# Kernel tuning notes

Hardware: AMD Instinct MI355X
Metric: run time of the kernel (lower is better)

## Reference

```python
import jax, jax.numpy as jnp
import numpy as np

B, N, E, H, L = 32, 128, 128, 8, 4      # graphs, nodes/graph, emb, heads, layers
ATOM, BOND, K, M = 64, 15, 32, 16384    # atom_dim, bond_dim, rbf_K, n_edges
CUTOFF = 5.0
DH = E // H


def _ln(x, g, b):
    mu = x.mean(-1, keepdims=True)
    var = ((x - mu) ** 2).mean(-1, keepdims=True)
    return (x - mu) / jnp.sqrt(var + 1e-5) * g + b


def setup_inputs() -> dict:
    key = jax.random.key(0)
    ks = iter(jax.random.split(key, 40))
    def rn(shape, s=1.0):
        return jax.random.normal(next(ks), shape, jnp.float32) * s
    inp = {}
    inp["x"] = rn((B * N, ATOM))
    inp["ei"] = jax.random.randint(next(ks), (2, M), 0, B * N, jnp.int32)
    bf = rn((M, BOND))
    dist = jax.random.uniform(next(ks), (M, 1), jnp.float32, 0.0, CUTOFF)
    inp["ea"] = jnp.concatenate([bf, dist], axis=1)  # last col = distance
    inp["pos"] = rn((B * N, 3), 2.0)
    inp["batch"] = jnp.repeat(jnp.arange(B, dtype=jnp.int32), N)  # contiguous equal-size graphs
    s = 0.02
    inp["Wproj"] = rn((ATOM, E), s); inp["bproj"] = jnp.zeros((E,), jnp.float32)
    EIN = BOND + K
    inp["Wlin"] = rn((EIN, E * E), s); inp["blin"] = jnp.zeros((E * E,), jnp.float32)
    inp["g_en"] = jnp.ones((E,), jnp.float32); inp["b_en"] = jnp.zeros((E,), jnp.float32)
    for nm in ["Wq", "Wk", "Wv", "Wo"]:
        inp[nm] = rn((L, E, E), s)
    for nm in ["bq", "bk", "bv", "bo"]:
        inp[nm] = jnp.zeros((L, E), jnp.float32)
    inp["g1"] = jnp.ones((L, E), jnp.float32); inp["b1"] = jnp.zeros((L, E), jnp.float32)
    inp["W1"] = rn((L, E, 2 * E), s); inp["bf1"] = jnp.zeros((L, 2 * E), jnp.float32)
    inp["W2"] = rn((L, 2 * E, E), s); inp["bf2"] = jnp.zeros((L, E), jnp.float32)
    inp["g2"] = jnp.ones((L, E), jnp.float32); inp["b2"] = jnp.zeros((L, E), jnp.float32)
    return inp


def reference(x, ei, ea, pos, batch, Wproj, bproj, Wlin, blin, g_en, b_en,
              Wq, bq, Wk, bk, Wv, bv, Wo, bo, g1, b1, W1, bf1, W2, bf2, g2, b2):
    # node projection
    h = x @ Wproj + bproj                              # [BN, E]
    # GaussianRBF on last edge-attr column
    d = jnp.clip(ea[:, -1], 0.0, 10.0)
    centers = jnp.linspace(0.0, CUTOFF, K)
    gamma = (CUTOFF / (K - 1)) ** -2
    rbf = jnp.exp(-gamma * (d[:, None] - centers) ** 2)  # [M, K]
    ea2 = jnp.concatenate([ea[:, :-1], rbf], axis=1)     # [M, BOND+K]
    # EdgeNetwork: gather -> per-edge matvec -> scatter-add -> LN
    m = (ea2 @ Wlin + blin).reshape(M, E, E)             # [M, E, E]
    msg = jnp.einsum('mef,mf->me', m, h[ei[1]])          # [M, E]
    agg = jnp.zeros_like(h).at[ei[0]].add(msg)
    h = _ln(h + agg, g_en, b_en)
    # batch-to-dense (equal-size contiguous graphs -> reshape)
    xp = h.reshape(B, N, E)
    pb = pos.reshape(B, N, 3)
    d2 = jnp.sum((pb[:, :, None, :] - pb[:, None, :, :]) ** 2, axis=-1)  # [B, N, N]
    db = jnp.where(d2 > 0, jnp.sqrt(jnp.where(d2 > 0, d2, 1.0)), 0.0)    # cdist
    mask = jnp.ones((B, N), bool)
    inv_sqrt_dh = 1.0 / np.sqrt(DH)
    for l in range(L):
        q = (xp @ Wq[l] + bq[l]).reshape(B, N, H, DH)
        k = (xp @ Wk[l] + bk[l]).reshape(B, N, H, DH)
        v = (xp @ Wv[l] + bv[l]).reshape(B, N, H, DH)
        sc = jnp.einsum('bihd,bjhd->bhij', q, k) * inv_sqrt_dh + db[:, None]
        sc = jnp.clip(sc, -10.0, 10.0)
        sc = jnp.where(mask[:, None, None, :], sc, -jnp.inf)
        a = jax.nn.softmax(sc, axis=-1)
        o = jnp.einsum('bhij,bjhd->bihd', a, v).reshape(B, N, E)
        att = o @ Wo[l] + bo[l]
        x1 = _ln(xp + att, g1[l], b1[l])
        ff = jax.nn.relu(x1 @ W1[l] + bf1[l]) @ W2[l] + bf2[l]
        xp = _ln(x1 + ff, g2[l], b2[l])
    mf = mask.astype(xp.dtype)[:, :, None]
    return (xp * mf).sum(1) / (mf.sum(1) + 1e-8)      # [B, E]
```

## Files before the change

kernel.cpp:

```cpp
#include <hip/hip_runtime.h>


typedef __attribute__((ext_vector_type(8))) short bf16x8;
typedef __attribute__((ext_vector_type(4))) float f32x4;
#define MFMA16(a, b, c) __builtin_amdgcn_mfma_f32_16x16x32_bf16(a, b, c, 0, 0, 0)

__device__ inline unsigned short f2bf(float f) {
  unsigned u = __float_as_uint(f);
  u = (u + 0x7FFF + ((u >> 16) & 1)) >> 16;
  return (unsigned short)u;
}
__device__ inline unsigned pack2(float a, float b) {
  return (unsigned)f2bf(a) | ((unsigned)f2bf(b) << 16);
}

__global__ __launch_bounds__(256) void k_setup(
    const float* __restrict__ x, const float* __restrict__ Wproj,
    const float* __restrict__ bproj, float* __restrict__ h,
    unsigned short* __restrict__ hb,
    const float* __restrict__ ea, float* __restrict__ ea2,
    const float* __restrict__ Wlin, const float* __restrict__ blin,
    unsigned short* __restrict__ wb,
    const float* __restrict__ Wq, const float* __restrict__ Wk,
    const float* __restrict__ Wv, const float* __restrict__ bq,
    const float* __restrict__ bk, const float* __restrict__ bv,
    unsigned short* __restrict__ qkvt, float* __restrict__ qkvb,
    const float* __restrict__ Wo, unsigned short* __restrict__ wot,
    const float* __restrict__ W1, unsigned short* __restrict__ w1t,
    const float* __restrict__ W2, unsigned short* __restrict__ w2t,
    float* __restrict__ agg,
    const float* __restrict__ pos, float* __restrict__ db) {
  __shared__ float xs[2][64];
  int blk = blockIdx.x, t = threadIdx.x;
  if (blk < 2048) {
    int sub = t >> 7, e = t & 127;
    int n = blk * 2 + sub;
    if (e < 64) xs[sub][e] = x[n * 64 + e];
    __syncthreads();
    float acc = bproj[e];
#pragma unroll
    for (int a = 0; a < 64; a++) acc += xs[sub][a] * Wproj[a * 128 + e];
    h[n * 128 + e] = acc;
    hb[n * 128 + e] = f2bf(acc);
    return;
  }
  int idx = (blk - 2048) * 256 + t;
  if (idx < 524288) { agg[idx] = 0.0f; return; }
  idx -= 524288;
  if (idx < 786432) {
    int m = idx / 48, c = idx % 48;
    float v;
    if (c < 15) {
      v = ea[m * 16 + c];
    } else if (c < 47) {
      int i = c - 15;
      float d = fminf(10.0f, fmaxf(0.0f, ea[m * 16 + 15]));
      float diff = d - 5.0f * (float)i / 31.0f;
      v = __expf(-38.44f * diff * diff);
    } else {
      v = 1.0f;
    }
    ea2[m * 48 + c] = v;
    return;
  }
  idx -= 786432;
  if (idx < 786432) {
    float v = (idx < 770048) ? Wlin[idx] : blin[idx - 770048];
    wb[idx] = f2bf(v);
    return;
  }
  idx -= 786432;
  if (idx < 196608) {
    int l = idx / 49152, r = idx % 49152;
    int j = r / 128, a = r % 128;
    int jj = j & 127;
    const float* W = (j < 128) ? Wq : (j < 256) ? Wk : Wv;
    qkvt[idx] = f2bf(W[l * 16384 + a * 128 + jj]);
    if (a == 0) {
      const float* bb = (j < 128) ? bq : (j < 256) ? bk : bv;
      qkvb[l * 384 + j] = bb[l * 128 + jj];
    }
    return;
  }
  idx -= 196608;
  if (idx < 65536) {
    int l = idx / 16384, r = idx % 16384;
    int a = r / 128, j = r % 128;
    wot[l * 16384 + j * 128 + a] = f2bf(Wo[idx]);
    return;
  }
  idx -= 65536;
  if (idx < 131072) {
    int l = idx / 32768, r = idx % 32768;
    int a = r / 256, j = r % 256;
    w1t[l * 32768 + j * 128 + a] = f2bf(W1[idx]);
    return;
  }
  idx -= 131072;
  if (idx < 131072) {
    int l = idx / 32768, r = idx % 32768;
    int a = r / 128, j = r % 128;
    w2t[l * 32768 + j * 256 + a] = f2bf(W2[idx]);
    return;
  }
  idx -= 131072;
  {
    int j = idx & 127, i2 = (idx >> 7) & 127, b = idx >> 14;
    float x0 = pos[(b * 128 + i2) * 3 + 0];
    float y0 = pos[(b * 128 + i2) * 3 + 1];
    float z0 = pos[(b * 128 + i2) * 3 + 2];
    float dx = x0 - pos[(b * 128 + j) * 3 + 0];
    float dy = y0 - pos[(b * 128 + j) * 3 + 1];
    float dz = z0 - pos[(b * 128 + j) * 3 + 2];
    float d2 = dx * dx + dy * dy + dz * dz;
    db[b * 16384 + i2 * 128 + j] = (d2 > 0.0f) ? sqrtf(d2) : 0.0f;
  }
}

__global__ __launch_bounds__(256) void k_edge(const float* __restrict__ ea2,
    const int* __restrict__ ei, const unsigned short* __restrict__ hbf,
    const unsigned short* __restrict__ wb, float* __restrict__ agg) {
  __shared__ unsigned short hs[8192];
  __shared__ float et[64][48];
  __shared__ unsigned short Bs[16384];
  __shared__ int srcs[64], dsts[64];
  int t = threadIdx.x, m0 = blockIdx.x * 64;
  if (t < 64) { srcs[t] = ei[16384 + m0 + t]; dsts[t] = ei[m0 + t]; }
  __syncthreads();
  uint4* hs4 = (uint4*)hs;
#pragma unroll
  for (int i = 0; i < 4; i++) {
    int q = t + i * 256;
    int row = q >> 4, ch = q & 15;
    hs4[row * 16 + (ch ^ (row & 7))] = ((const uint4*)(hbf + (size_t)srcs[row] * 128))[ch];
  }
#pragma unroll
  for (int i = 0; i < 12; i++) {
    int p = t + i * 256;
    int mi = p / 48, c = p % 48;
    et[mi][c] = ea2[(size_t)(m0 + mi) * 48 + c];
  }
  int w = t >> 6, l = t & 63, lr = l & 15, lg = l >> 4;
  float msg[2][4][4] = {};
  const f32x4 zf = {0.f, 0.f, 0.f, 0.f};
  uint4* Bs4 = (uint4*)Bs;
  for (int c = 0; c < 48; c++) {
    __syncthreads();
#pragma unroll
    for (int i = 0; i < 8; i++) {
      int q = t + i * 256;
      int row = q >> 4, ch = q & 15;
      Bs4[row * 16 + (ch ^ (row & 7))] =
          ((const uint4*)(wb + (size_t)c * 16384 + row * 128))[ch];
    }
    __syncthreads();
    f32x4 pacc[2][4];
#pragma unroll
    for (int s = 0; s < 4; s++) {
      bf16x8 af[2];
#pragma unroll
      for (int e2 = 0; e2 < 2; e2++) {
        int er = w * 32 + e2 * 16 + lr;
        int ch = (s * 4 + lg) ^ (er & 7);
        af[e2] = *(const bf16x8*)&Bs[(er * 16 + ch) * 8];
      }
#pragma unroll
      for (int n = 0; n < 4; n++) {
        int nr = n * 16 + lr;
        int ch = (s * 4 + lg) ^ (nr & 7);
        bf16x8 bfr = *(const bf16x8*)&hs[(nr * 16 + ch) * 8];
        if (s == 0) {
          pacc[0][n] = MFMA16(af[0], bfr, zf);
          pacc[1][n] = MFMA16(af[1], bfr, zf);
        } else {
          pacc[0][n] = MFMA16(af[0], bfr, pacc[0][n]);
          pacc[1][n] = MFMA16(af[1], bfr, pacc[1][n]);
        }
      }
    }
#pragma unroll
    for (int n = 0; n < 4; n++) {
      float am = et[n * 16 + lr][c];
#pragma unroll
      for (int e2 = 0; e2 < 2; e2++)
#pragma unroll
        for (int r = 0; r < 4; r++)
          msg[e2][n][r] += am * pacc[e2][n][r];
    }
  }
#pragma unroll
  for (int n = 0; n < 4; n++) {
    int dst = dsts[n * 16 + lr];
#pragma unroll
    for (int e2 = 0; e2 < 2; e2++) {
      int e0 = w * 32 + e2 * 16 + lg * 4;
#pragma unroll
      for (int r = 0; r < 4; r++)
        atomicAdd(&agg[(size_t)dst * 128 + e0 + r], msg[e2][n][r]);
    }
  }
}

__global__ __launch_bounds__(256) void k_lnqkv(const float* __restrict__ agg,
    const float* __restrict__ hbuf, const float* __restrict__ g_en,
    const float* __restrict__ b_en, float* __restrict__ xp,
    const unsigned short* __restrict__ qkvt, const float* __restrict__ qkvb,
    float* __restrict__ qkv) {
  __shared__ unsigned short As[8192];
  __shared__ unsigned short Bs[16384];
  int t = threadIdx.x, m0 = blockIdx.x * 64;
  int w = t >> 6, l = t & 63, lr = l & 15, lg = l >> 4;
  float ge0 = g_en[2 * l], ge1 = g_en[2 * l + 1];
  float be0 = b_en[2 * l], be1 = b_en[2 * l + 1];
  for (int i = 0; i < 16; i++) {
    int r = i * 4 + w;
    float2 av = ((const float2*)(agg + (size_t)(m0 + r) * 128))[l];
    float2 hv = ((const float2*)(hbuf + (size_t)(m0 + r) * 128))[l];
    float v0 = av.x + hv.x, v1 = av.y + hv.y;
    float s = v0 + v1, s2 = v0 * v0 + v1 * v1;
#pragma unroll
    for (int o = 1; o < 64; o <<= 1) { s += __shfl_xor(s, o); s2 += __shfl_xor(s2, o); }
    float mu = s * (1.0f / 128.0f);
    float var = fmaxf(s2 * (1.0f / 128.0f) - mu * mu, 0.0f);
    float inv = rsqrtf(var + 1e-5f);
    float o0 = (v0 - mu) * inv * ge0 + be0;
    float o1 = (v1 - mu) * inv * ge1 + be1;
    ((float2*)(xp + (size_t)(m0 + r) * 128))[l] = make_float2(o0, o1);
    ((unsigned*)As)[(r * 16 + ((l >> 2) ^ (r & 7))) * 4 + (l & 3)] = pack2(o0, o1);
  }
  uint4* Bs4 = (uint4*)Bs;
  for (int cchunk = 0; cchunk < 3; cchunk++) {
    __syncthreads();
#pragma unroll
    for (int i = 0; i < 8; i++) {
      int q = t + i * 256;
      int row = q >> 4, ch = q & 15;
      Bs4[row * 16 + (ch ^ (row & 7))] =
          ((const uint4*)(qkvt + (size_t)(cchunk * 128 + row) * 128))[ch];
    }
    __syncthreads();
    f32x4 acc[2][4];
#pragma unroll
    for (int e2 = 0; e2 < 2; e2++)
#pragma unroll
      for (int n = 0; n < 4; n++) acc[e2][n] = (f32x4){0.f, 0.f, 0.f, 0.f};
#pragma unroll
    for (int s = 0; s < 4; s++) {
      bf16x8 af[2];
#pragma unroll
      for (int e2 = 0; e2 < 2; e2++) {
        int er = w * 32 + e2 * 16 + lr;
        int ch = (s * 4 + lg) ^ (er & 7);
        af[e2] = *(const bf16x8*)&Bs[(er * 16 + ch) * 8];
      }
#pragma unroll
      for (int n = 0; n < 4; n++) {
        int nr = n * 16 + lr;
        int ch = (s * 4 + lg) ^ (nr & 7);
        bf16x8 bfr = *(const bf16x8*)&As[(nr * 16 + ch) * 8];
        acc[0][n] = MFMA16(af[0], bfr, acc[0][n]);
        acc[1][n] = MFMA16(af[1], bfr, acc[1][n]);
      }
    }
#pragma unroll
    for (int e2 = 0; e2 < 2; e2++) {
      int e0 = cchunk * 128 + w * 32 + e2 * 16 + lg * 4;
      float4 bb = *(const float4*)&qkvb[e0];
#pragma unroll
      for (int n = 0; n < 4; n++) {
        int node = m0 + n * 16 + lr;
        float4 ov;
#pragma unroll
        for (int r = 0; r < 4; r++) ((float*)&ov)[r] = acc[e2][n][r] + ((const float*)&bb)[r];
        *(float4*)&qkv[(size_t)node * 384 + e0] = ov;
      }
    }
  }
}

__global__ __launch_bounds__(128) void k_attn(const float* __restrict__ qkv,
    const float* __restrict__ db, float* __restrict__ oatt) {
  __shared__ float ks[128][16], vs[128][16];
  int bh = blockIdx.x, b = bh >> 3, h = bh & 7;
  int i = threadIdx.x;
  int node = b * 128 + i;
  const float4* kr = (const float4*)(qkv + (size_t)node * 384 + 128 + h * 16);
  const float4* vr = (const float4*)(qkv + (size_t)node * 384 + 256 + h * 16);
#pragma unroll
  for (int d4 = 0; d4 < 4; d4++) {
    *(float4*)&ks[i][d4 * 4] = kr[d4];
    *(float4*)&vs[i][d4 * 4] = vr[d4];
  }
  float qr[16];
  const float4* qp = (const float4*)(qkv + (size_t)node * 384 + h * 16);
#pragma unroll
  for (int d4 = 0; d4 < 4; d4++) *(float4*)&qr[d4 * 4] = qp[d4];
  __syncthreads();
  const float4* dbr = (const float4*)(db + b * 16384 + i * 128);
  float rsum = 0.0f, o[16] = {};
  for (int j4 = 0; j4 < 32; j4++) {
    float4 dv = dbr[j4];
#pragma unroll
    for (int u = 0; u < 4; u++) {
      int j = j4 * 4 + u;
      float s = 0.0f;
#pragma unroll
      for (int d = 0; d < 16; d++) s += qr[d] * ks[j][d];
      s = s * 0.25f + ((const float*)&dv)[u];
      s = fminf(10.0f, fmaxf(-10.0f, s));
      float p = __expf(s);
      rsum += p;
#pragma unroll
      for (int d = 0; d < 16; d++) o[d] += p * vs[j][d];
    }
  }
  float r = 1.0f / rsum;
  float* op = oatt + (size_t)node * 128 + h * 16;
#pragma unroll
  for (int d4 = 0; d4 < 4; d4++)
    *(float4*)&op[d4 * 4] = make_float4(o[d4 * 4] * r, o[d4 * 4 + 1] * r, o[d4 * 4 + 2] * r, o[d4 * 4 + 3] * r);
}

template <int QKV>
__global__ __launch_bounds__(256) void k_loqkv(
    const float* __restrict__ oatt, float* __restrict__ xp,
    const unsigned short* __restrict__ wot, const float* __restrict__ bo,
    const float* __restrict__ g1, const float* __restrict__ b1,
    const unsigned short* __restrict__ w1t, const float* __restrict__ bf1,
    const unsigned short* __restrict__ w2t, const float* __restrict__ bf2,
    const float* __restrict__ g2, const float* __restrict__ b2,
    const unsigned short* __restrict__ qkvtn, const float* __restrict__ qkvbn,
    float* __restrict__ qkv) {
  __shared__ unsigned short ffs[16384];
  __shared__ unsigned short x1s[8192];
  __shared__ unsigned short Bs[16384];
  __shared__ float red[2][4][64];
  int t = threadIdx.x;
  int m0 = blockIdx.x << 6;
  int w = t >> 6, l = t & 63, lr = l & 15, lg = l >> 4;

  {
    uint4* a4 = (uint4*)ffs;
#pragma unroll
    for (int i = 0; i < 4; i++) {
      int q = t + i * 256;
      int row = q >> 4, ch = q & 15;
      const float* ap = oatt + (size_t)(m0 + row) * 128 + ch * 8;
      float4 fa = *(const float4*)ap;
      float4 fb = *(const float4*)(ap + 4);
      uint4 pk;
      pk.x = pack2(fa.x, fa.y); pk.y = pack2(fa.z, fa.w);
      pk.z = pack2(fb.x, fb.y); pk.w = pack2(fb.z, fb.w);
      a4[row * 16 + (ch ^ (row & 7))] = pk;
    }
    uint4* b4p = (uint4*)Bs;
#pragma unroll
    for (int i = 0; i < 8; i++) {
      int q = t + i * 256;
      int row = q >> 4, ch = q & 15;
      b4p[row * 16 + (ch ^ (row & 7))] = *((const uint4*)(wot + (size_t)row * 128) + ch);
    }
  }
  __syncthreads();
  f32x4 acc[2][4];
#pragma unroll
  for (int et = 0; et < 2; et++)
#pragma unroll
    for (int n = 0; n < 4; n++) acc[et][n] = (f32x4){0.f, 0.f, 0.f, 0.f};
#pragma unroll
  for (int s = 0; s < 4; s++) {
    bf16x8 af[2];
#pragma unroll
    for (int et = 0; et < 2; et++) {
      int er = w * 32 + et * 16 + lr;
      int ch = (s * 4 + lg) ^ (er & 7);
      af[et] = *(const bf16x8*)&Bs[(er * 16 + ch) * 8];
    }
#pragma unroll
    for (int n = 0; n < 4; n++) {
      int nr = n * 16 + lr;
      int ch = (s * 4 + lg) ^ (nr & 7);
      bf16x8 bfr = *(const bf16x8*)&ffs[(nr * 16 + ch) * 8];
      acc[0][n] = MFMA16(af[0], bfr, acc[0][n]);
      acc[1][n] = MFMA16(af[1], bfr, acc[1][n]);
    }
  }
  float v1[2][4][4];
  {
    int e0 = w * 32 + lg * 4;
    float4 bo4[2] = { *(const float4*)&bo[e0], *(const float4*)&bo[e0 + 16] };
#pragma unroll
    for (int et = 0; et < 2; et++)
#pragma unroll
      for (int n = 0; n < 4; n++) {
        int node = m0 + n * 16 + lr;
        float4 rv = *(const float4*)&xp[(size_t)node * 128 + e0 + et * 16];
#pragma unroll
        for (int r = 0; r < 4; r++)
          v1[et][n][r] = acc[et][n][r] + ((const float*)&bo4[et])[r] + ((const float*)&rv)[r];
      }
    float s[4], s2[4];
#pragma unroll
    for (int n = 0; n < 4; n++) {
      float a = 0, b2s = 0;
#pragma unroll
      for (int et = 0; et < 2; et++)
#pragma unroll
        for (int r = 0; r < 4; r++) { a += v1[et][n][r]; b2s += v1[et][n][r] * v1[et][n][r]; }
      s[n] = a; s2[n] = b2s;
    }
#pragma unroll
    for (int off = 16; off < 64; off <<= 1)
#pragma unroll
      for (int n = 0; n < 4; n++) { s[n] += __shfl_xor(s[n], off); s2[n] += __shfl_xor(s2[n], off); }
    if (l < 16) {
#pragma unroll
      for (int n = 0; n < 4; n++) { red[0][w][n * 16 + lr] = s[n]; red[1][w][n * 16 + lr] = s2[n]; }
    }
    __syncthreads();
    float4 g4[2] = { *(const float4*)&g1[e0], *(const float4*)&g1[e0 + 16] };
    float4 bb4[2] = { *(const float4*)&b1[e0], *(const float4*)&b1[e0 + 16] };
#pragma unroll
    for (int n = 0; n < 4; n++) {
      int nloc = n * 16 + lr;
      float ts  = red[0][0][nloc] + red[0][1][nloc] + red[0][2][nloc] + red[0][3][nloc];
      float ts2 = red[1][0][nloc] + red[1][1][nloc] + red[1][2][nloc] + red[1][3][nloc];
      float mu = ts * (1.0f / 128.0f);
      float var = fmaxf(ts2 * (1.0f / 128.0f) - mu * mu, 0.0f);
      float inv = rsqrtf(var + 1e-5f);
#pragma unroll
      for (int et = 0; et < 2; et++) {
#pragma unroll
        for (int r = 0; r < 4; r++)
          v1[et][n][r] = (v1[et][n][r] - mu) * inv * ((const float*)&g4[et])[r] + ((const float*)&bb4[et])[r];
        int ch = w * 4 + et * 2 + (lg >> 1);
        uint2 pk;
        pk.x = pack2(v1[et][n][0], v1[et][n][1]);
        pk.y = pack2(v1[et][n][2], v1[et][n][3]);
        *(uint2*)&x1s[(nloc * 16 + (ch ^ (nloc & 7))) * 8 + (lg & 1) * 4] = pk;
      }
    }
  }
  __syncthreads();

  for (int ct = 0; ct < 2; ct++) {
    if (ct) __syncthreads();
    uint4* b4p = (uint4*)Bs;
#pragma unroll
    for (int i = 0; i < 8; i++) {
      int q = t + i * 256;
      int row = q >> 4, ch = q & 15;
      b4p[row * 16 + (ch ^ (row & 7))] =
          *((const uint4*)(w1t + (size_t)(ct * 128 + row) * 128) + ch);
    }
    __syncthreads();
#pragma unroll
    for (int et = 0; et < 2; et++)
#pragma unroll
      for (int n = 0; n < 4; n++) acc[et][n] = (f32x4){0.f, 0.f, 0.f, 0.f};
#pragma unroll
    for (int s = 0; s < 4; s++) {
      bf16x8 af[2];
#pragma unroll
      for (int et = 0; et < 2; et++) {
        int er = w * 32 + et * 16 + lr;
        int ch = (s * 4 + lg) ^ (er & 7);
        af[et] = *(const bf16x8*)&Bs[(er * 16 + ch) * 8];
      }
#pragma unroll
      for (int n = 0; n < 4; n++) {
        int nr = n * 16 + lr;
        int ch = (s * 4 + lg) ^ (nr & 7);
        bf16x8 bfr = *(const bf16x8*)&x1s[(nr * 16 + ch) * 8];
        acc[0][n] = MFMA16(af[0], bfr, acc[0][n]);
        acc[1][n] = MFMA16(af[1], bfr, acc[1][n]);
      }
    }
    int e0 = w * 32 + lg * 4;
    float4 bb0 = *(const float4*)&bf1[ct * 128 + e0];
    float4 bb1 = *(const float4*)&bf1[ct * 128 + e0 + 16];
#pragma unroll
    for (int et = 0; et < 2; et++) {
      const float* bbp = et ? (const float*)&bb1 : (const float*)&bb0;
#pragma unroll
      for (int n = 0; n < 4; n++) {
        int nloc = n * 16 + lr;
        float f0 = fmaxf(acc[et][n][0] + bbp[0], 0.0f);
        float f1 = fmaxf(acc[et][n][1] + bbp[1], 0.0f);
        float f2 = fmaxf(acc[et][n][2] + bbp[2], 0.0f);
        float f3 = fmaxf(acc[et][n][3] + bbp[3], 0.0f);
        int cg = ct * 16 + w * 4 + et * 2 + (lg >> 1);
        uint2 pk;
        pk.x = pack2(f0, f1);
        pk.y = pack2(f2, f3);
        *(uint2*)&ffs[(nloc * 32 + (cg ^ (nloc & 7))) * 8 + (lg & 1) * 4] = pk;
      }
    }
  }
  __syncthreads();

  f32x4 acc3[2][4];
#pragma unroll
  for (int et = 0; et < 2; et++)
#pragma unroll
    for (int n = 0; n < 4; n++) acc3[et][n] = (f32x4){0.f, 0.f, 0.f, 0.f};
  for (int kc = 0; kc < 2; kc++) {
    if (kc) __syncthreads();
    uint4* b4p = (uint4*)Bs;
#pragma unroll
    for (int i = 0; i < 8; i++) {
      int q = t + i * 256;
      int row = q >> 4, ch = q & 15;
      b4p[row * 16 + (ch ^ (row & 7))] =
          *((const uint4*)(w2t + (size_t)row * 256 + kc * 128) + ch);
    }
    __syncthreads();
#pragma unroll
    for (int s = 0; s < 4; s++) {
      bf16x8 af[2];
#pragma unroll
      for (int et = 0; et < 2; et++) {
        int er = w * 32 + et * 16 + lr;
        int ch = (s * 4 + lg) ^ (er & 7);
        af[et] = *(const bf16x8*)&Bs[(er * 16 + ch) * 8];
      }
#pragma unroll
      for (int n = 0; n < 4; n++) {
        int nr = n * 16 + lr;
        int gch = kc * 16 + s * 4 + lg;
        bf16x8 bfr = *(const bf16x8*)&ffs[(nr * 32 + (gch ^ (nr & 7))) * 8];
        acc3[0][n] = MFMA16(af[0], bfr, acc3[0][n]);
        acc3[1][n] = MFMA16(af[1], bfr, acc3[1][n]);
      }
    }
  }
  {
    int e0 = w * 32 + lg * 4;
    float4 bo4[2] = { *(const float4*)&bf2[e0], *(const float4*)&bf2[e0 + 16] };
    float v2[2][4][4];
#pragma unroll
    for (int et = 0; et < 2; et++)
#pragma unroll
      for (int n = 0; n < 4; n++)
#pragma unroll
        for (int r = 0; r < 4; r++)
          v2[et][n][r] = acc3[et][n][r] + ((const float*)&bo4[et])[r] + v1[et][n][r];
    float s[4], s2[4];
#pragma unroll
    for (int n = 0; n < 4; n++) {
      float a = 0, b2s = 0;
#pragma unroll
      for (int et = 0; et < 2; et++)
#pragma unroll
        for (int r = 0; r < 4; r++) { a += v2[et][n][r]; b2s += v2[et][n][r] * v2[et][n][r]; }
      s[n] = a; s2[n] = b2s;
    }
#pragma unroll
    for (int off = 16; off < 64; off <<= 1)
#pragma unroll
      for (int n = 0; n < 4; n++) { s[n] += __shfl_xor(s[n], off); s2[n] += __shfl_xor(s2[n], off); }
    __syncthreads();
    if (l < 16) {
#pragma unroll
      for (int n = 0; n < 4; n++) { red[0][w][n * 16 + lr] = s[n]; red[1][w][n * 16 + lr] = s2[n]; }
    }
    __syncthreads();
    float4 g4[2] = { *(const float4*)&g2[e0], *(const float4*)&g2[e0 + 16] };
    float4 bb4[2] = { *(const float4*)&b2[e0], *(const float4*)&b2[e0 + 16] };
#pragma unroll
    for (int n = 0; n < 4; n++) {
      int nloc = n * 16 + lr;
      float ts  = red[0][0][nloc] + red[0][1][nloc] + red[0][2][nloc] + red[0][3][nloc];
      float ts2 = red[1][0][nloc] + red[1][1][nloc] + red[1][2][nloc] + red[1][3][nloc];
      float mu = ts * (1.0f / 128.0f);
      float var = fmaxf(ts2 * (1.0f / 128.0f) - mu * mu, 0.0f);
      float inv = rsqrtf(var + 1e-5f);
      int node = m0 + nloc;
#pragma unroll
      for (int et = 0; et < 2; et++) {
        float4 ov;
#pragma unroll
        for (int r = 0; r < 4; r++)
          ((float*)&ov)[r] = (v2[et][n][r] - mu) * inv * ((const float*)&g4[et])[r] + ((const float*)&bb4[et])[r];
        *(float4*)&xp[(size_t)node * 128 + e0 + et * 16] = ov;
        if (QKV) {
          int ch = w * 4 + et * 2 + (lg >> 1);
          uint2 pk;
          pk.x = pack2(((float*)&ov)[0], ((float*)&ov)[1]);
          pk.y = pack2(((float*)&ov)[2], ((float*)&ov)[3]);
          *(uint2*)&x1s[(nloc * 16 + (ch ^ (nloc & 7))) * 8 + (lg & 1) * 4] = pk;
        }
      }
    }
  }

  if (QKV) {
    uint4* Bs4 = (uint4*)Bs;
    for (int cchunk = 0; cchunk < 3; cchunk++) {
      __syncthreads();
#pragma unroll
      for (int i = 0; i < 8; i++) {
        int q = t + i * 256;
        int row = q >> 4, ch = q & 15;
        Bs4[row * 16 + (ch ^ (row & 7))] =
            ((const uint4*)(qkvtn + (size_t)(cchunk * 128 + row) * 128))[ch];
      }
      __syncthreads();
      f32x4 qa[2][4];
#pragma unroll
      for (int e2 = 0; e2 < 2; e2++)
#pragma unroll
        for (int n = 0; n < 4; n++) qa[e2][n] = (f32x4){0.f, 0.f, 0.f, 0.f};
#pragma unroll
      for (int s = 0; s < 4; s++) {
        bf16x8 af[2];
#pragma unroll
        for (int e2 = 0; e2 < 2; e2++) {
          int er = w * 32 + e2 * 16 + lr;
          int ch = (s * 4 + lg) ^ (er & 7);
          af[e2] = *(const bf16x8*)&Bs[(er * 16 + ch) * 8];
        }
#pragma unroll
        for (int n = 0; n < 4; n++) {
          int nr = n * 16 + lr;
          int ch = (s * 4 + lg) ^ (nr & 7);
          bf16x8 bfr = *(const bf16x8*)&x1s[(nr * 16 + ch) * 8];
          qa[0][n] = MFMA16(af[0], bfr, qa[0][n]);
          qa[1][n] = MFMA16(af[1], bfr, qa[1][n]);
        }
      }
#pragma unroll
      for (int e2 = 0; e2 < 2; e2++) {
        int e0 = cchunk * 128 + w * 32 + e2 * 16 + lg * 4;
        float4 bb = *(const float4*)&qkvbn[e0];
#pragma unroll
        for (int n = 0; n < 4; n++) {
          int node = m0 + n * 16 + lr;
          float4 ov;
#pragma unroll
          for (int r = 0; r < 4; r++) ((float*)&ov)[r] = qa[e2][n][r] + ((const float*)&bb)[r];
          *(float4*)&qkv[(size_t)node * 384 + e0] = ov;
        }
      }
    }
  }
}

__global__ __launch_bounds__(128) void k_pool(const float* __restrict__ xp, float* __restrict__ out) {
  int b = blockIdx.x, e = threadIdx.x;
  float s = 0.0f;
  for (int n = 0; n < 128; n++) s += xp[(b * 128 + n) * 128 + e];
  out[b * 128 + e] = s * (1.0f / 128.0f);
}

extern "C" void kernel_launch(void* const* d_in, const int* in_sizes, int n_in,
                              void* d_out, int out_size, void* d_ws, size_t ws_size,
                              hipStream_t stream) {
  const float* x     = (const float*)d_in[0];
  const int*   ei    = (const int*)  d_in[1];
  const float* ea    = (const float*)d_in[2];
  const float* pos   = (const float*)d_in[3];
  const float* Wproj = (const float*)d_in[5];
  const float* bproj = (const float*)d_in[6];
  const float* Wlin  = (const float*)d_in[7];
  const float* blin  = (const float*)d_in[8];
  const float* g_en  = (const float*)d_in[9];
  const float* b_en  = (const float*)d_in[10];
  const float* Wq    = (const float*)d_in[11];
  const float* Wk    = (const float*)d_in[12];
  const float* Wv    = (const float*)d_in[13];
  const float* Wo    = (const float*)d_in[14];
  const float* bq    = (const float*)d_in[15];
  const float* bk    = (const float*)d_in[16];
  const float* bv    = (const float*)d_in[17];
  const float* bo    = (const float*)d_in[18];
  const float* g1    = (const float*)d_in[19];
  const float* b1    = (const float*)d_in[20];
  const float* W1    = (const float*)d_in[21];
  const float* bf1   = (const float*)d_in[22];
  const float* W2    = (const float*)d_in[23];
  const float* bf2   = (const float*)d_in[24];
  const float* g2    = (const float*)d_in[25];
  const float* b2    = (const float*)d_in[26];

  float* ws = (float*)d_ws;
  float* ea2  = ws;
  float* hbuf = ea2  + 786432;
  float* agg  = hbuf + 524288;
  unsigned short* hbf  = (unsigned short*)(agg + 524288);
  unsigned short* wbf  = hbf + 524288;
  unsigned short* qkvt = wbf + 786432;
  unsigned short* wot  = qkvt + 196608;
  unsigned short* w1t  = wot + 65536;
  unsigned short* w2t  = w1t + 131072;
  float* qkvb = (float*)(w2t + 131072);
  float* db   = qkvb + 1536;
  float* xp   = db   + 524288;
  float* qkv  = xp   + 524288;
  float* oatt = qkv  + 1572864;

  k_setup<<<14336, 256, 0, stream>>>(x, Wproj, bproj, hbuf, hbf,
      ea, ea2, Wlin, blin, wbf, Wq, Wk, Wv, bq, bk, bv, qkvt, qkvb,
      Wo, wot, W1, w1t, W2, w2t, agg, pos, db);
  k_edge<<<256, 256, 0, stream>>>(ea2, ei, hbf, wbf, agg);
  k_lnqkv<<<64, 256, 0, stream>>>(agg, hbuf, g_en, b_en, xp, qkvt, qkvb, qkv);

  for (int l = 0; l < 4; l++) {
    k_attn<<<256, 128, 0, stream>>>(qkv, db, oatt);
    if (l < 3) {
      k_loqkv<1><<<64, 256, 0, stream>>>(oatt, xp,
          wot + l * 16384, bo + l * 128, g1 + l * 128, b1 + l * 128,
          w1t + l * 32768, bf1 + l * 256,
          w2t + l * 32768, bf2 + l * 128, g2 + l * 128, b2 + l * 128,
          qkvt + (l + 1) * 49152, qkvb + (l + 1) * 384, qkv);
    } else {
      k_loqkv<0><<<64, 256, 0, stream>>>(oatt, xp,
          wot + l * 16384, bo + l * 128, g1 + l * 128, b1 + l * 128,
          w1t + l * 32768, bf1 + l * 256,
          w2t + l * 32768, bf2 + l * 128, g2 + l * 128, b2 + l * 128,
          nullptr, nullptr, nullptr);
    }
  }

  k_pool<<<32, 128, 0, stream>>>(xp, (float*)d_out);
}
```

Before: 380.8 us.

## Reassociate edge network: precompute per-node transforms, then contract per edge

Replaces the fused per-edge kernel with two kernels. k_tbuild computes T[node][c] = Wlin_c·h for every node with MFMA, and k_contract then gathers T for each edge's source and dots it with the edge features before atomically adding into agg. The aim is to stop recomputing the 48 channel matmuls once per edge, since there are more edges than nodes. In exchange it writes and re-reads a large bf16 intermediate (about 50 MB) with gathered reads, and the extra bf16 rounding adds error. The intermediate reuses the qkv/oatt workspace region.

```diff
diff --git a/kernel.cpp b/kernel.cpp
--- a/kernel.cpp
+++ b/kernel.cpp
@@ -12,6 +12,9 @@
 }
 __device__ inline unsigned pack2(float a, float b) {
   return (unsigned)f2bf(a) | ((unsigned)f2bf(b) << 16);
+}
+__device__ inline float bf2f(unsigned short v) {
+  return __uint_as_float(((unsigned)v) << 16);
 }
 
 __global__ __launch_bounds__(256) void k_setup(
@@ -117,88 +120,77 @@
   }
 }
 
-__global__ __launch_bounds__(256) void k_edge(const float* __restrict__ ea2,
-    const int* __restrict__ ei, const unsigned short* __restrict__ hbf,
-    const unsigned short* __restrict__ wb, float* __restrict__ agg) {
-  __shared__ unsigned short hs[8192];
-  __shared__ float et[64][48];
-  __shared__ unsigned short Bs[16384];
-  __shared__ int srcs[64], dsts[64];
-  int t = threadIdx.x, m0 = blockIdx.x * 64;
-  if (t < 64) { srcs[t] = ei[16384 + m0 + t]; dsts[t] = ei[m0 + t]; }
-  __syncthreads();
+__global__ __launch_bounds__(256) void k_tbuild(const unsigned short* __restrict__ hb,
+    const unsigned short* __restrict__ wb, unsigned short* __restrict__ T) {
+  __shared__ unsigned short hs[16384];
+  __shared__ unsigned short wsm[16384];
+  int c = blockIdx.x >> 5;
+  int n0 = (blockIdx.x & 31) << 7;
+  int t = threadIdx.x;
+  const uint4* hg = (const uint4*)hb + n0 * 16;
+  const uint4* wg = (const uint4*)wb + c * 2048;
   uint4* hs4 = (uint4*)hs;
-#pragma unroll
-  for (int i = 0; i < 4; i++) {
+  uint4* ws4 = (uint4*)wsm;
+#pragma unroll
+  for (int i = 0; i < 8; i++) {
     int q = t + i * 256;
     int row = q >> 4, ch = q & 15;
-    hs4[row * 16 + (ch ^ (row & 7))] = ((const uint4*)(hbf + (size_t)srcs[row] * 128))[ch];
-  }
-#pragma unroll
-  for (int i = 0; i < 12; i++) {
-    int p = t + i * 256;
-    int mi = p / 48, c = p % 48;
-    et[mi][c] = ea2[(size_t)(m0 + mi) * 48 + c];
-  }
-  int w = t >> 6, l = t & 63, lr = l & 15, lg = l >> 4;
-  float msg[2][4][4] = {};
-  const f32x4 zf = {0.f, 0.f, 0.f, 0.f};
-  uint4* Bs4 = (uint4*)Bs;
-  for (int c = 0; c < 48; c++) {
-    __syncthreads();
-#pragma unroll
-    for (int i = 0; i < 8; i++) {
-      int q = t + i * 256;
-      int row = q >> 4, ch = q & 15;
-      Bs4[row * 16 + (ch ^ (row & 7))] =
-          ((const uint4*)(wb + (size_t)c * 16384 + row * 128))[ch];
-    }
-    __syncthreads();
-    f32x4 pacc[2][4];
-#pragma unroll
-    for (int s = 0; s < 4; s++) {
-      bf16x8 af[2];
-#pragma unroll
-      for (int e2 = 0; e2 < 2; e2++) {
-        int er = w * 32 + e2 * 16 + lr;
-        int ch = (s * 4 + lg) ^ (er & 7);
-        af[e2] = *(const bf16x8*)&Bs[(er * 16 + ch) * 8];
-      }
-#pragma unroll
-      for (int n = 0; n < 4; n++) {
-        int nr = n * 16 + lr;
-        int ch = (s * 4 + lg) ^ (nr & 7);
-        bf16x8 bfr = *(const bf16x8*)&hs[(nr * 16 + ch) * 8];
-        if (s == 0) {
-          pacc[0][n] = MFMA16(af[0], bfr, zf);
-          pacc[1][n] = MFMA16(af[1], bfr, zf);
-        } else {
-          pacc[0][n] = MFMA16(af[0], bfr, pacc[0][n]);
-          pacc[1][n] = MFMA16(af[1], bfr, pacc[1][n]);
-        }
-      }
-    }
-#pragma unroll
-    for (int n = 0; n < 4; n++) {
-      float am = et[n * 16 + lr][c];
-#pragma unroll
-      for (int e2 = 0; e2 < 2; e2++)
-#pragma unroll
-        for (int r = 0; r < 4; r++)
-          msg[e2][n][r] += am * pacc[e2][n][r];
-    }
-  }
-#pragma unroll
-  for (int n = 0; n < 4; n++) {
-    int dst = dsts[n * 16 + lr];
-#pragma unroll
-    for (int e2 = 0; e2 < 2; e2++) {
-      int e0 = w * 32 + e2 * 16 + lg * 4;
-#pragma unroll
-      for (int r = 0; r < 4; r++)
-        atomicAdd(&agg[(size_t)dst * 128 + e0 + r], msg[e2][n][r]);
-    }
-  }
+    int d = row * 16 + (ch ^ (row & 7));
+    hs4[d] = hg[q];
+    ws4[d] = wg[q];
+  }
+  __syncthreads();
+  int w = t >> 6, l = t & 63;
+  int lr = l & 15, lg = l >> 4;
+  f32x4 acc[2][8];
+#pragma unroll
+  for (int et = 0; et < 2; et++)
+#pragma unroll
+    for (int n = 0; n < 8; n++) acc[et][n] = (f32x4){0.f, 0.f, 0.f, 0.f};
+#pragma unroll
+  for (int s = 0; s < 4; s++) {
+    bf16x8 af[2];
+#pragma unroll
+    for (int et = 0; et < 2; et++) {
+      int er = w * 32 + et * 16 + lr;
+      int ch = (s * 4 + lg) ^ (er & 7);
+      af[et] = *(const bf16x8*)&wsm[(er * 16 + ch) * 8];
+    }
+#pragma unroll
+    for (int n = 0; n < 8; n++) {
+      int nr = n * 16 + lr;
+      int ch = (s * 4 + lg) ^ (nr & 7);
+      bf16x8 bfr = *(const bf16x8*)&hs[(nr * 16 + ch) * 8];
+      acc[0][n] = MFMA16(af[0], bfr, acc[0][n]);
+      acc[1][n] = MFMA16(af[1], bfr, acc[1][n]);
+    }
+  }
+#pragma unroll
+  for (int et = 0; et < 2; et++)
+#pragma unroll
+    for (int n = 0; n < 8; n++) {
+      int node = n0 + n * 16 + lr;
+      int e0 = w * 32 + et * 16 + lg * 4;
+      uint2 pk;
+      pk.x = pack2(acc[et][n][0], acc[et][n][1]);
+      pk.y = pack2(acc[et][n][2], acc[et][n][3]);
+      *(uint2*)&T[node * 6144 + c * 128 + e0] = pk;
+    }
+}
+
+__global__ __launch_bounds__(128) void k_contract(const float* __restrict__ ea2,
+    const int* __restrict__ ei, const unsigned short* __restrict__ T,
+    float* __restrict__ agg) {
+  int m = blockIdx.x, e = threadIdx.x;
+  int src = ei[16384 + m], dst = ei[m];
+  __shared__ float ec[48];
+  if (e < 48) ec[e] = ea2[m * 48 + e];
+  __syncthreads();
+  const unsigned short* Ts = T + src * 6144;
+  float acc = 0.0f;
+#pragma unroll 6
+  for (int c = 0; c < 48; c++) acc += ec[c] * bf2f(Ts[c * 128 + e]);
+  atomicAdd(&agg[dst * 128 + e], acc);
 }
 
 __global__ __launch_bounds__(256) void k_lnqkv(const float* __restrict__ agg,
@@ -696,13 +688,16 @@
   float* qkvb = (float*)(w2t + 131072);
   float* db   = qkvb + 1536;
   float* xp   = db   + 524288;
-  float* qkv  = xp   + 524288;
-  float* oatt = qkv  + 1572864;
+  float* Tf = xp + 524288;
+  unsigned short* Tb = (unsigned short*)Tf;
+  float* qkv  = Tf;
+  float* oatt = qkv + 1572864;
 
   k_setup<<<14336, 256, 0, stream>>>(x, Wproj, bproj, hbuf, hbf,
       ea, ea2, Wlin, blin, wbf, Wq, Wk, Wv, bq, bk, bv, qkvt, qkvb,
       Wo, wot, W1, w1t, W2, w2t, agg, pos, db);
-  k_edge<<<256, 256, 0, stream>>>(ea2, ei, hbf, wbf, agg);
+  k_tbuild<<<1536, 256, 0, stream>>>(hbf, wbf, Tb);
+  k_contract<<<16384, 128, 0, stream>>>(ea2, ei, Tb, agg);
   k_lnqkv<<<64, 256, 0, stream>>>(agg, hbuf, g_en, b_en, xp, qkvt, qkvb, qkv);
 
   for (int l = 0; l < 4; l++) {
```

Result: faster. 341.8 us (-10.2%).
